# Kernel optimization log

Hardware: AMD Instinct MI355X
Metric: run time of the kernel (lower is better)

Reference implementation:

```python
import jax, jax.numpy as jnp
import numpy as np

N = 100000      # nodes
E = 1600000     # graph edges (avg degree 16)
Q = 1000000     # query edges to score
IN, HID, OUT = 128, 128, 64


def setup_inputs() -> dict:
    key = jax.random.key(0)
    ks = jax.random.split(key, 7)
    feat = jax.random.normal(ks[0], (N, IN), dtype=jnp.float32)
    edge_src = jax.random.randint(ks[1], (E,), 0, N, dtype=jnp.int32)
    edge_dst = jax.random.randint(ks[2], (E,), 0, N, dtype=jnp.int32)
    src = jax.random.randint(ks[3], (Q,), 0, N, dtype=jnp.int32)
    dst = jax.random.randint(ks[4], (Q,), 0, N, dtype=jnp.int32)
    W1 = jax.random.normal(ks[5], (IN, HID), dtype=jnp.float32) / np.sqrt(IN).astype(np.float32)
    b1 = jnp.zeros((HID,), jnp.float32)
    W2 = jax.random.normal(ks[6], (HID, OUT), dtype=jnp.float32) / np.sqrt(HID).astype(np.float32)
    b2 = jnp.zeros((OUT,), jnp.float32)
    return {"feat": feat, "edge_src": edge_src, "edge_dst": edge_dst,
            "src": src, "dst": dst, "W1": W1, "b1": b1, "W2": W2, "b2": b2}


def _graph_conv(h, W, b, edge_src, edge_dst, out_norm, in_norm):
    """DGL GraphConv(norm='both'): D_out^{-1/2} -> aggregate -> D_in^{-1/2}, W, b.
    DGL applies W before aggregation when in_feats > out_feats (same math)."""
    n = h.shape[0]
    h = h * out_norm[:, None]
    if h.shape[1] > W.shape[1]:
        h = h @ W
        agg = jax.ops.segment_sum(h[edge_src], edge_dst, num_segments=n)
    else:
        agg = jax.ops.segment_sum(h[edge_src], edge_dst, num_segments=n)
        agg = agg @ W
    return agg * in_norm[:, None] + b


def reference(feat, edge_src, edge_dst, src, dst, W1, b1, W2, b2):
    n = feat.shape[0]
    ones = jnp.ones((edge_src.shape[0],), feat.dtype)
    out_deg = jax.ops.segment_sum(ones, edge_src, num_segments=n)
    in_deg = jax.ops.segment_sum(ones, edge_dst, num_segments=n)
    out_norm = jnp.maximum(out_deg, 1.0) ** -0.5
    in_norm = jnp.maximum(in_deg, 1.0) ** -0.5

    h = _graph_conv(feat, W1, b1, edge_src, edge_dst, out_norm, in_norm)
    h = jax.nn.relu(h)  # dropout is identity at inference
    h = _graph_conv(h, W2, b2, edge_src, edge_dst, out_norm, in_norm)

    edge_scores = jnp.sum(h[src] * h[dst], axis=-1)
    return jax.nn.sigmoid(edge_scores)
```

## Files before the change

kernel.cpp:

```cpp
#include <hip/hip_runtime.h>
#include <math.h>

static inline size_t align256(size_t x) { return (x + 255) & ~(size_t)255; }

typedef __attribute__((ext_vector_type(8))) short bf16x8;
typedef __attribute__((ext_vector_type(4))) float f32x4;
typedef __attribute__((ext_vector_type(2))) float f32x2;
typedef __attribute__((ext_vector_type(2))) _Float16 half2_t;

__device__ inline float bfLo(unsigned int u) {
  union { unsigned int i; float f; } v; v.i = u << 16; return v.f;
}
__device__ inline float bfHi(unsigned int u) {
  union { unsigned int i; float f; } v; v.i = u & 0xffff0000u; return v.f;
}
__device__ inline unsigned short f2bf(float f) {
  union { float f; unsigned int i; } v; v.f = f;
  unsigned int r = v.i + 0x7FFF + ((v.i >> 16) & 1);
  return (unsigned short)(r >> 16);
}
__device__ inline unsigned int packbf(float lo, float hi) {
  return ((unsigned int)f2bf(hi) << 16) | f2bf(lo);
}
__device__ inline unsigned int packh(float lo, float hi) {
  union { _Float16 h[2]; unsigned int u; } v;
  v.h[0] = (_Float16)lo; v.h[1] = (_Float16)hi;
  return v.u;
}
__device__ inline float qdot(unsigned int a, unsigned int b, float acc) {
#if __has_builtin(__builtin_amdgcn_fdot2)
  union { unsigned int u; half2_t h; } va, vb;
  va.u = a; vb.u = b;
  return __builtin_amdgcn_fdot2(va.h, vb.h, acc, false);
#else
  union { unsigned int u; _Float16 h[2]; } va, vb;
  va.u = a; vb.u = b;
  return acc + (float)va.h[0] * (float)vb.h[0] + (float)va.h[1] * (float)vb.h[1];
#endif
}

__global__ __launch_bounds__(256) void k_coarse_count(const int* __restrict__ esrc,
                                                      const int* __restrict__ edst,
                                                      int E, int chunk, int NB, int G,
                                                      int* __restrict__ blkD,
                                                      int* __restrict__ blkS,
                                                      const float* __restrict__ W1,
                                                      const float* __restrict__ W2,
                                                      unsigned short* __restrict__ W1t,
                                                      unsigned short* __restrict__ W2t) {
  __shared__ int hD[512], hS[512];
  int blk = blockIdx.x, tid = threadIdx.x;
  int t = blk * 256 + tid;
  if (t < 128 * 128) {
    int nn = t >> 7, kk = t & 127;
    W1t[t] = f2bf(W1[kk * 128 + nn]);
  }
  if (t < 64 * 128) {
    int nn = t >> 7, kk = t & 127;
    W2t[t] = f2bf(W2[kk * 64 + nn]);
  }
  for (int i = tid; i < NB; i += 256) { hD[i] = 0; hS[i] = 0; }
  __syncthreads();
  int s0 = blk * chunk, s1 = min(E, s0 + chunk);
  for (int e = s0 + tid; e < s1; e += 256) {
    atomicAdd(&hD[edst[e] >> 8], 1);
    atomicAdd(&hS[esrc[e] >> 8], 1);
  }
  __syncthreads();
  for (int i = tid; i < NB; i += 256) {
    blkD[i * G + blk] = hD[i];
    blkS[i * G + blk] = hS[i];
  }
}

__global__ __launch_bounds__(256) void k_scan1(const int* __restrict__ in,
                                               int* __restrict__ out,
                                               int* __restrict__ bsums, int n) {
  __shared__ int s[256];
  int tid = threadIdx.x, gid = blockIdx.x * 256 + tid;
  int v = (gid < n) ? in[gid] : 0;
  s[tid] = v; __syncthreads();
  for (int o = 1; o < 256; o <<= 1) {
    int t = (tid >= o) ? s[tid - o] : 0;
    __syncthreads();
    s[tid] += t;
    __syncthreads();
  }
  if (gid < n) out[gid] = s[tid] - v;
  if (tid == 255) bsums[blockIdx.x] = s[255];
}

__global__ __launch_bounds__(512) void k_scan2(int* __restrict__ bsums, int nb) {
  __shared__ int s[512];
  int tid = threadIdx.x;
  int* base = bsums + blockIdx.x * nb;
  int v = (tid < nb) ? base[tid] : 0;
  s[tid] = v; __syncthreads();
  for (int o = 1; o < 512; o <<= 1) {
    int t = (tid >= o) ? s[tid - o] : 0;
    __syncthreads();
    s[tid] += t;
    __syncthreads();
  }
  if (tid < nb) base[tid] = s[tid] - v;
}

__global__ __launch_bounds__(256) void k_coarse_scatter(const int* __restrict__ esrc,
                                                        const int* __restrict__ edst,
                                                        int E, int chunk, int NB, int G,
                                                        const int* __restrict__ scD,
                                                        const int* __restrict__ scS,
                                                        const int* __restrict__ bsums,
                                                        unsigned int* __restrict__ pairs,
                                                        unsigned int* __restrict__ keys) {
  __shared__ int cD[512], cS[512];
  int blk = blockIdx.x, tid = threadIdx.x;
  for (int i = tid; i < NB; i += 256) {
    cD[i] = scD[i * G + blk] + bsums[i];
    cS[i] = scS[i * G + blk] + bsums[NB + i];
  }
  __syncthreads();
  int s0 = blk * chunk, s1 = min(E, s0 + chunk);
  for (int e = s0 + tid; e < s1; e += 256) {
    int s = esrc[e], d = edst[e];
    int pd = atomicAdd(&cD[d >> 8], 1);
    pairs[pd] = ((unsigned)s << 8) | ((unsigned)d & 255u);
    int ps = atomicAdd(&cS[s >> 8], 1);
    keys[ps] = (unsigned)s;
  }
}

__global__ __launch_bounds__(256) void k_fine(const unsigned int* __restrict__ pairs,
                                              const unsigned int* __restrict__ keys,
                                              const int* __restrict__ scD,
                                              const int* __restrict__ scS,
                                              const int* __restrict__ bsums,
                                              int G, int E, int N, int NB,
                                              int* __restrict__ cntIn,
                                              float* __restrict__ normIn,
                                              int* __restrict__ offs,
                                              int* __restrict__ csr,
                                              float* __restrict__ normOut) {
  __shared__ int hist[256], scn[256], cur[256];
  int tid = threadIdx.x;
  if (blockIdx.x >= (unsigned)NB) {
    int b = blockIdx.x - NB;
    int bstart = scS[b * G] + bsums[NB + b];
    int bend = (b + 1 < NB) ? scS[(b + 1) * G] + bsums[NB + b + 1] : E;
    hist[tid] = 0;
    __syncthreads();
    for (int e = bstart + tid; e < bend; e += 256)
      atomicAdd(&hist[keys[e] & 255u], 1);
    __syncthreads();
    int node = b * 256 + tid;
    if (node < N) normOut[node] = rsqrtf((float)max(hist[tid], 1));
    return;
  }
  int b = blockIdx.x;
  int bstart = scD[b * G] + bsums[b];
  int bend = (b + 1 < NB) ? scD[(b + 1) * G] + bsums[b + 1] : E;
  hist[tid] = 0;
  __syncthreads();
  for (int e = bstart + tid; e < bend; e += 256)
    atomicAdd(&hist[pairs[e] & 255u], 1);
  __syncthreads();
  int v = hist[tid];
  scn[tid] = v;
  __syncthreads();
  for (int o = 1; o < 256; o <<= 1) {
    int t = (tid >= o) ? scn[tid - o] : 0;
    __syncthreads();
    scn[tid] += t;
    __syncthreads();
  }
  int excl = scn[tid] - v;
  cur[tid] = excl;
  int node = b * 256 + tid;
  if (node < N) {
    cntIn[node] = v;
    normIn[node] = rsqrtf((float)max(v, 1));
    offs[node] = bstart + excl;
  }
  __syncthreads();
  for (int e = bstart + tid; e < bend; e += 256) {
    unsigned int u = pairs[e];
    int p = bstart + atomicAdd(&cur[u & 255u], 1);
    csr[p] = (int)(u >> 8);
  }
}

template <int C, typename TA>
__global__ __launch_bounds__(256) void k_mgemm(const TA* __restrict__ A,
                                               const float* __restrict__ scale,
                                               const unsigned short* __restrict__ Wt,
                                               unsigned short* __restrict__ out, int n) {
  constexpr int KP = 136;
  constexpr int NCH = C / 16;
  __shared__ __align__(16) unsigned short Al[64 * KP];
  __shared__ __align__(16) unsigned short Wl[C * KP];
  int tid = threadIdx.x;
  int r0 = blockIdx.x * 64;

  {
    const uint4* Wg = (const uint4*)Wt;
    uint4* Wd = (uint4*)Wl;
    for (int idx = tid; idx < C * 16; idx += 256) {
      int row = idx >> 4, seg = idx & 15;
      Wd[row * 17 + seg] = Wg[idx];
    }
  }
  {
    int seg = tid & 7;
    for (int it = 0; it < 2; ++it) {
      int row = (tid >> 3) + it * 32;
      int g = r0 + row;
      float v[16];
      if (g < n) {
        float sc = scale[g];
        if constexpr (sizeof(TA) == 4) {
          const float4* Ag = (const float4*)((const float*)A + (size_t)g * 128);
#pragma unroll
          for (int j = 0; j < 4; ++j) {
            float4 f = Ag[seg * 4 + j];
            v[j * 4 + 0] = f.x * sc; v[j * 4 + 1] = f.y * sc;
            v[j * 4 + 2] = f.z * sc; v[j * 4 + 3] = f.w * sc;
          }
        } else {
          const uint4* Ag = (const uint4*)((const unsigned short*)A + (size_t)g * 128);
#pragma unroll
          for (int j = 0; j < 2; ++j) {
            uint4 u = Ag[seg * 2 + j];
            v[j * 8 + 0] = bfLo(u.x) * sc; v[j * 8 + 1] = bfHi(u.x) * sc;
            v[j * 8 + 2] = bfLo(u.y) * sc; v[j * 8 + 3] = bfHi(u.y) * sc;
            v[j * 8 + 4] = bfLo(u.z) * sc; v[j * 8 + 5] = bfHi(u.z) * sc;
            v[j * 8 + 6] = bfLo(u.w) * sc; v[j * 8 + 7] = bfHi(u.w) * sc;
          }
        }
      } else {
#pragma unroll
        for (int j = 0; j < 16; ++j) v[j] = 0.f;
      }
      uint4* dst = (uint4*)(Al + row * KP + seg * 16);
      dst[0] = make_uint4(packbf(v[0], v[1]), packbf(v[2], v[3]),
                          packbf(v[4], v[5]), packbf(v[6], v[7]));
      dst[1] = make_uint4(packbf(v[8], v[9]), packbf(v[10], v[11]),
                          packbf(v[12], v[13]), packbf(v[14], v[15]));
    }
  }
  __syncthreads();

  int lane = tid & 63;
  int w = tid >> 6;
  int quad = lane >> 4, m16 = lane & 15;
  f32x4 acc[NCH];
#pragma unroll
  for (int c = 0; c < NCH; ++c) acc[c] = (f32x4){0.f, 0.f, 0.f, 0.f};

#pragma unroll
  for (int kc = 0; kc < 4; ++kc) {
    int ko = kc * 32 + quad * 8;
    bf16x8 a = *(const bf16x8*)(Al + (w * 16 + m16) * KP + ko);
#pragma unroll
    for (int c = 0; c < NCH; ++c) {
      bf16x8 b = *(const bf16x8*)(Wl + (c * 16 + m16) * KP + ko);
      acc[c] = __builtin_amdgcn_mfma_f32_16x16x32_bf16(a, b, acc[c], 0, 0, 0);
    }
  }

#pragma unroll
  for (int c = 0; c < NCH; ++c)
#pragma unroll
    for (int r = 0; r < 4; ++r) {
      int g = r0 + w * 16 + quad * 4 + r;
      if (g < n) out[(size_t)g * C + c * 16 + m16] = f2bf(acc[c][r]);
    }
}

__global__ __launch_bounds__(256) void k_agg128_relu(const unsigned short* __restrict__ X,
                                                     const int* __restrict__ csr,
                                                     const int* __restrict__ offs,
                                                     const int* __restrict__ cnt,
                                                     const float* __restrict__ norm,
                                                     const float* __restrict__ bias,
                                                     unsigned short* __restrict__ H, int n) {
  int wid = blockIdx.x * 4 + (threadIdx.x >> 6);
  if (wid >= n) return;
  int lane = threadIdx.x & 63;
  int sub = lane & 15;
  int grp = lane >> 4;
  int start = offs[wid], m = cnt[wid];
  const int* p = csr + start;
  const uint4* Xv = (const uint4*)X;
  f32x2 a0 = {0.f, 0.f}, a1 = {0.f, 0.f}, a2 = {0.f, 0.f}, a3 = {0.f, 0.f};
  for (int c0 = 0; c0 < m; c0 += 64) {
    int take = min(64, m - c0);
    int iv = p[c0 + ((lane < take) ? lane : take - 1)];
    int e = 0;
    for (; e + 16 <= take; e += 16) {
      uint4 uu[4];
#pragma unroll
      for (int j = 0; j < 4; ++j) {
        int ss = __shfl(iv, e + j * 4 + grp);
        uu[j] = Xv[(size_t)ss * 16 + sub];
      }
#pragma unroll
      for (int j = 0; j < 4; ++j) {
        a0 += (f32x2){bfLo(uu[j].x), bfHi(uu[j].x)};
        a1 += (f32x2){bfLo(uu[j].y), bfHi(uu[j].y)};
        a2 += (f32x2){bfLo(uu[j].z), bfHi(uu[j].z)};
        a3 += (f32x2){bfLo(uu[j].w), bfHi(uu[j].w)};
      }
    }
    for (; e + 4 <= take; e += 4) {
      int ss = __shfl(iv, e + grp);
      uint4 u = Xv[(size_t)ss * 16 + sub];
      a0 += (f32x2){bfLo(u.x), bfHi(u.x)};
      a1 += (f32x2){bfLo(u.y), bfHi(u.y)};
      a2 += (f32x2){bfLo(u.z), bfHi(u.z)};
      a3 += (f32x2){bfLo(u.w), bfHi(u.w)};
    }
    int r = take - e;
    if (r > 0) {
      int ss = __shfl(iv, min(e + grp, take - 1));
      uint4 u = Xv[(size_t)ss * 16 + sub];
      if (grp < r) {
        a0 += (f32x2){bfLo(u.x), bfHi(u.x)};
        a1 += (f32x2){bfLo(u.y), bfHi(u.y)};
        a2 += (f32x2){bfLo(u.z), bfHi(u.z)};
        a3 += (f32x2){bfLo(u.w), bfHi(u.w)};
      }
    }
  }
  float a[8] = {a0.x, a0.y, a1.x, a1.y, a2.x, a2.y, a3.x, a3.y};
#pragma unroll
  for (int k = 0; k < 8; ++k) {
    a[k] += __shfl_xor(a[k], 16);
    a[k] += __shfl_xor(a[k], 32);
  }
  float nm = norm[wid];
  const float4* bv = (const float4*)bias;
  float4 b0 = bv[sub * 2], b1 = bv[sub * 2 + 1];
  if (grp == 0) {
    float o0 = fmaxf(a[0] * nm + b0.x, 0.f);
    float o1 = fmaxf(a[1] * nm + b0.y, 0.f);
    float o2 = fmaxf(a[2] * nm + b0.z, 0.f);
    float o3 = fmaxf(a[3] * nm + b0.w, 0.f);
    float o4 = fmaxf(a[4] * nm + b1.x, 0.f);
    float o5 = fmaxf(a[5] * nm + b1.y, 0.f);
    float o6 = fmaxf(a[6] * nm + b1.z, 0.f);
    float o7 = fmaxf(a[7] * nm + b1.w, 0.f);
    uint4 o = make_uint4(packbf(o0, o1), packbf(o2, o3),
                         packbf(o4, o5), packbf(o6, o7));
    ((uint4*)H)[(size_t)wid * 16 + sub] = o;
  }
}

__global__ __launch_bounds__(256) void k_agg64(const unsigned short* __restrict__ X,
                                               const int* __restrict__ csr,
                                               const int* __restrict__ offs,
                                               const int* __restrict__ cnt,
                                               const float* __restrict__ norm,
                                               const float* __restrict__ bias,
                                               unsigned short* __restrict__ H, int n) {
  int wid = blockIdx.x * 4 + (threadIdx.x >> 6);
  if (wid >= n) return;
  int lane = threadIdx.x & 63;
  int sub = lane & 7;
  int grp = lane >> 3;
  int start = offs[wid], m = cnt[wid];
  const int* p = csr + start;
  const uint4* Xv = (const uint4*)X;
  f32x2 a0 = {0.f, 0.f}, a1 = {0.f, 0.f}, a2 = {0.f, 0.f}, a3 = {0.f, 0.f};
  for (int c0 = 0; c0 < m; c0 += 64) {
    int take = min(64, m - c0);
    int iv = p[c0 + ((lane < take) ? lane : take - 1)];
    int e = 0;
    for (; e + 32 <= take; e += 32) {
      uint4 uu[4];
#pragma unroll
      for (int j = 0; j < 4; ++j) {
        int ss = __shfl(iv, e + j * 8 + grp);
        uu[j] = Xv[(size_t)ss * 8 + sub];
      }
#pragma unroll
      for (int j = 0; j < 4; ++j) {
        a0 += (f32x2){bfLo(uu[j].x), bfHi(uu[j].x)};
        a1 += (f32x2){bfLo(uu[j].y), bfHi(uu[j].y)};
        a2 += (f32x2){bfLo(uu[j].z), bfHi(uu[j].z)};
        a3 += (f32x2){bfLo(uu[j].w), bfHi(uu[j].w)};
      }
    }
    for (; e + 8 <= take; e += 8) {
      int ss = __shfl(iv, e + grp);
      uint4 u = Xv[(size_t)ss * 8 + sub];
      a0 += (f32x2){bfLo(u.x), bfHi(u.x)};
      a1 += (f32x2){bfLo(u.y), bfHi(u.y)};
      a2 += (f32x2){bfLo(u.z), bfHi(u.z)};
      a3 += (f32x2){bfLo(u.w), bfHi(u.w)};
    }
    int r = take - e;
    if (r > 0) {
      int ss = __shfl(iv, min(e + grp, take - 1));
      uint4 u = Xv[(size_t)ss * 8 + sub];
      if (grp < r) {
        a0 += (f32x2){bfLo(u.x), bfHi(u.x)};
        a1 += (f32x2){bfLo(u.y), bfHi(u.y)};
        a2 += (f32x2){bfLo(u.z), bfHi(u.z)};
        a3 += (f32x2){bfLo(u.w), bfHi(u.w)};
      }
    }
  }
  float a[8] = {a0.x, a0.y, a1.x, a1.y, a2.x, a2.y, a3.x, a3.y};
#pragma unroll
  for (int k = 0; k < 8; ++k) {
    a[k] += __shfl_xor(a[k], 8);
    a[k] += __shfl_xor(a[k], 16);
    a[k] += __shfl_xor(a[k], 32);
  }
  float nm = norm[wid];
  const float4* bv = (const float4*)bias;
  float4 b0 = bv[sub * 2], b1 = bv[sub * 2 + 1];
  if (grp == 0) {
    uint4 o = make_uint4(packh(a[0] * nm + b0.x, a[1] * nm + b0.y),
                         packh(a[2] * nm + b0.z, a[3] * nm + b0.w),
                         packh(a[4] * nm + b1.x, a[5] * nm + b1.y),
                         packh(a[6] * nm + b1.z, a[7] * nm + b1.w));
    ((uint4*)H)[(size_t)wid * 8 + sub] = o;
  }
}

__global__ __launch_bounds__(256) void k_score(const unsigned short* __restrict__ H,
                                               const int* __restrict__ qs,
                                               const int* __restrict__ qd,
                                               float* __restrict__ out, int q, int qStride) {
  int t = blockIdx.x * 256 + threadIdx.x;
  int sub = t & 7;
  int q0 = t >> 3;
  int q1 = q0 + qStride;
  const uint4* Hv = (const uint4*)H;
  float p0 = 0.f, p1 = 0.f;
  if (q0 < q) {
    uint4 a = Hv[(size_t)qs[q0] * 8 + sub];
    uint4 b = Hv[(size_t)qd[q0] * 8 + sub];
    uint4 c, d;
    bool has1 = (q1 < q);
    if (has1) {
      c = Hv[(size_t)qs[q1] * 8 + sub];
      d = Hv[(size_t)qd[q1] * 8 + sub];
    }
    p0 = qdot(a.x, b.x, p0); p0 = qdot(a.y, b.y, p0);
    p0 = qdot(a.z, b.z, p0); p0 = qdot(a.w, b.w, p0);
    if (has1) {
      p1 = qdot(c.x, d.x, p1); p1 = qdot(c.y, d.y, p1);
      p1 = qdot(c.z, d.z, p1); p1 = qdot(c.w, d.w, p1);
    }
  }
  p0 += __shfl_xor(p0, 1); p1 += __shfl_xor(p1, 1);
  p0 += __shfl_xor(p0, 2); p1 += __shfl_xor(p1, 2);
  p0 += __shfl_xor(p0, 4); p1 += __shfl_xor(p1, 4);
  if (sub == 0 && q0 < q) {
    out[q0] = 1.f / (1.f + expf(-p0));
    if (q1 < q) out[q1] = 1.f / (1.f + expf(-p1));
  }
}

extern "C" void kernel_launch(void* const* d_in, const int* in_sizes, int n_in,
                              void* d_out, int out_size, void* d_ws, size_t ws_size,
                              hipStream_t stream) {
  const float* feat = (const float*)d_in[0];
  const int* esrc   = (const int*)d_in[1];
  const int* edst   = (const int*)d_in[2];
  const int* qsrc   = (const int*)d_in[3];
  const int* qdst   = (const int*)d_in[4];
  const float* W1   = (const float*)d_in[5];
  const float* b1   = (const float*)d_in[6];
  const float* W2   = (const float*)d_in[7];
  const float* b2   = (const float*)d_in[8];
  float* out = (float*)d_out;

  const int N = in_sizes[0] / 128;
  const int E = in_sizes[1];
  const int Q = in_sizes[3];

  const int G = 256;
  const int NB = (N + 255) >> 8;
  const int chunk = (E + G - 1) / G;
  const int lenS = NB * G;
  const int gScan = lenS / 256;

  char* w = (char*)d_ws;
  size_t o = 0;
  unsigned short* X1 = (unsigned short*)(w + o); o += align256((size_t)N * 128 * 2);
  unsigned short* X2 = (unsigned short*)(w + o); o += align256((size_t)N * 64 * 2);
  unsigned short* H2 = (unsigned short*)(w + o); o += align256((size_t)N * 64 * 2);
  int* cntIn = (int*)(w + o);       o += align256((size_t)N * 4);
  float* normOut = (float*)(w + o); o += align256((size_t)N * 4);
  float* normIn = (float*)(w + o);  o += align256((size_t)N * 4);
  int* offs = (int*)(w + o);        o += align256((size_t)N * 4);
  int* blk = (int*)(w + o);         o += align256((size_t)lenS * 8);
  int* sc = (int*)(w + o);          o += align256((size_t)lenS * 8);
  int* bsums = (int*)(w + o);       o += align256((size_t)8192);
  unsigned short* W1t = (unsigned short*)(w + o); o += align256((size_t)128 * 128 * 2);
  unsigned short* W2t = (unsigned short*)(w + o); o += align256((size_t)64 * 128 * 2);
  unsigned int* pairs = (unsigned int*)(w + o); o += align256((size_t)E * 4);
  unsigned int* keys = (unsigned int*)(w + o); o += align256((size_t)E * 4);
  int* csr = (int*)(w + o);         o += align256((size_t)E * 4);

  int* blkD = blk;        int* blkS = blk + lenS;
  int* scD = sc;          int* scS = sc + lenS;

  k_coarse_count<<<G, 256, 0, stream>>>(esrc, edst, E, chunk, NB, G, blkD, blkS,
                                        W1, W2, W1t, W2t);
  k_scan1<<<2 * gScan, 256, 0, stream>>>(blk, sc, bsums, 2 * lenS);
  k_scan2<<<2, 512, 0, stream>>>(bsums, gScan);
  k_coarse_scatter<<<G, 256, 0, stream>>>(esrc, edst, E, chunk, NB, G, scD, scS,
                                          bsums, pairs, keys);
  k_fine<<<2 * NB, 256, 0, stream>>>(pairs, keys, scD, scS, bsums, G, E, N, NB,
                                     cntIn, normIn, offs, csr, normOut);

  const int gRows = (N + 63) / 64;
  k_mgemm<128, float><<<gRows, 256, 0, stream>>>(feat, normOut, W1t, X1, N);
  k_agg128_relu<<<(N + 3) / 4, 256, 0, stream>>>(X1, csr, offs, cntIn, normIn, b1, X2, N);
  k_mgemm<64, unsigned short><<<gRows, 256, 0, stream>>>(X2, normOut, W2t, X1, N);
  k_agg64<<<(N + 3) / 4, 256, 0, stream>>>(X1, csr, offs, cntIn, normIn, b2, H2, N);
  const int qHalf = (Q + 1) / 2;
  k_score<<<((qHalf * 8) + 255) / 256, 256, 0, stream>>>(H2, qsrc, qdst, out, Q, qHalf);
}
```

Baseline: 318.8 us.

## Aggregate 128-wide layer via MFMA with mask matrix over 16-node groups

Replaces the per-node wave gather-and-add aggregation for layer one with a kernel where each wave handles 16 consecutive destination nodes. It streams their contiguous CSR neighbor rows through LDS in tiles of 32, reads them back with transposing LDS loads, and accumulates with bf16 MFMA using a 0/1 mask matrix that selects which edges belong to which node. This trades scalar FP adds and cross-lane reductions for matrix ops and wider coalesced loads. The cost is extra LDS traffic and wasted MFMA work on masked entries. Nodes beyond the last multiple of 16 (N>>4) are never processed, which is fine for N=100000 but not in general.

After: 324.7 us. About the same (+1.9%).

```diff
diff --git a/kernel.cpp b/kernel.cpp
--- a/kernel.cpp
+++ b/kernel.cpp
@@ -4,6 +4,7 @@
 static inline size_t align256(size_t x) { return (x + 255) & ~(size_t)255; }
 
 typedef __attribute__((ext_vector_type(8))) short bf16x8;
+typedef __attribute__((ext_vector_type(4))) short s16x4;
 typedef __attribute__((ext_vector_type(4))) float f32x4;
 typedef __attribute__((ext_vector_type(2))) float f32x2;
 typedef __attribute__((ext_vector_type(2))) _Float16 half2_t;
@@ -276,82 +277,108 @@
     }
 }
 
-__global__ __launch_bounds__(256) void k_agg128_relu(const unsigned short* __restrict__ X,
+__global__ __launch_bounds__(256) void k_agg128_mfma(const unsigned short* __restrict__ X,
                                                      const int* __restrict__ csr,
                                                      const int* __restrict__ offs,
                                                      const int* __restrict__ cnt,
                                                      const float* __restrict__ norm,
                                                      const float* __restrict__ bias,
-                                                     unsigned short* __restrict__ H, int n) {
-  int wid = blockIdx.x * 4 + (threadIdx.x >> 6);
-  if (wid >= n) return;
-  int lane = threadIdx.x & 63;
-  int sub = lane & 15;
-  int grp = lane >> 4;
-  int start = offs[wid], m = cnt[wid];
-  const int* p = csr + start;
-  const uint4* Xv = (const uint4*)X;
-  f32x2 a0 = {0.f, 0.f}, a1 = {0.f, 0.f}, a2 = {0.f, 0.f}, a3 = {0.f, 0.f};
-  for (int c0 = 0; c0 < m; c0 += 64) {
-    int take = min(64, m - c0);
-    int iv = p[c0 + ((lane < take) ? lane : take - 1)];
-    int e = 0;
-    for (; e + 16 <= take; e += 16) {
-      uint4 uu[4];
-#pragma unroll
-      for (int j = 0; j < 4; ++j) {
-        int ss = __shfl(iv, e + j * 4 + grp);
-        uu[j] = Xv[(size_t)ss * 16 + sub];
+                                                     unsigned short* __restrict__ H,
+                                                     int n, int E) {
+  __shared__ __attribute__((aligned(128))) unsigned short sA[4][32 * 128];
+  const int tid = threadIdx.x;
+  const int w = tid >> 6, l = tid & 63;
+  const int g = blockIdx.x * 4 + w;
+  const int nGroups = n >> 4;
+  if (g >= nGroups) return;
+  const int n0 = g << 4;
+
+  const int mnode = n0 + (l & 15);
+  const int s_m = offs[mnode];
+  const int c_m = cnt[mnode];
+  const int gs = __shfl(s_m, 0);
+  const int ge = __shfl(s_m + c_m, 15);
+  const int nt = (ge - gs + 31) >> 5;
+
+  const unsigned ldsb = (unsigned)(size_t)(&sA[w][0]);
+  unsigned short* ldsw = &sA[w][0];
+
+  const int eloc = (l >> 1) & 3;
+  const unsigned cbyte = (unsigned)(((l >> 3) << 5) | ((l & 1) << 4));
+
+  f32x4 acc[8];
+#pragma unroll
+  for (int c = 0; c < 8; ++c) acc[c] = (f32x4){0.f, 0.f, 0.f, 0.f};
+
+  const int kgrp = (l >> 4) << 3;
+  int ev = 0;
+  if (nt > 0) ev = csr[min(gs + (l & 31), E - 1)];
+
+  for (int t = 0; t < nt; ++t) {
+    const int tbase = gs + (t << 5);
+    uint4 st[8];
+#pragma unroll
+    for (int i = 0; i < 8; ++i) {
+      int row = __shfl(ev, (i << 2) + eloc);
+      st[i] = *(const uint4*)((const char*)X + ((size_t)(unsigned)row << 8) + cbyte);
+    }
+    if (t + 1 < nt) ev = csr[min(tbase + 32 + (l & 31), E - 1)];
+#pragma unroll
+    for (int i = 0; i < 8; ++i)
+      *(uint4*)((char*)ldsw + (i << 10) + (l << 4)) = st[i];
+
+    const int r0 = tbase + kgrp - s_m;
+    unsigned mw0 = (((unsigned)(r0 + 0) < (unsigned)c_m) ? 0x3F80u : 0u) |
+                   ((((unsigned)(r0 + 1) < (unsigned)c_m) ? 0x3F80u : 0u) << 16);
+    unsigned mw1 = (((unsigned)(r0 + 2) < (unsigned)c_m) ? 0x3F80u : 0u) |
+                   ((((unsigned)(r0 + 3) < (unsigned)c_m) ? 0x3F80u : 0u) << 16);
+    unsigned mw2 = (((unsigned)(r0 + 4) < (unsigned)c_m) ? 0x3F80u : 0u) |
+                   ((((unsigned)(r0 + 5) < (unsigned)c_m) ? 0x3F80u : 0u) << 16);
+    unsigned mw3 = (((unsigned)(r0 + 6) < (unsigned)c_m) ? 0x3F80u : 0u) |
+                   ((((unsigned)(r0 + 7) < (unsigned)c_m) ? 0x3F80u : 0u) << 16);
+    union { unsigned u[4]; bf16x8 v; } cv;
+    cv.u[0] = mw0; cv.u[1] = mw1; cv.u[2] = mw2; cv.u[3] = mw3;
+    const bf16x8 amask = cv.v;
+
+    asm volatile("s_waitcnt lgkmcnt(0)" ::: "memory");
+    __builtin_amdgcn_sched_barrier(0);
+
+    const unsigned ta = ldsb + (unsigned)(((l >> 4) << 11) + ((l & 15) << 3));
+    s16x4 lo[8], hi[8];
+#pragma unroll
+    for (int c = 0; c < 8; ++c) {
+      asm volatile("ds_read_b64_tr_b16 %0, %2 offset:0\n\t"
+                   "ds_read_b64_tr_b16 %1, %2 offset:1024"
+                   : "=v"(lo[c]), "=v"(hi[c])
+                   : "v"(ta + (unsigned)(c << 7)));
+    }
+    asm volatile("s_waitcnt lgkmcnt(0)" ::: "memory");
+    __builtin_amdgcn_sched_barrier(0);
+
+#pragma unroll
+    for (int c = 0; c < 8; ++c) {
+      bf16x8 b = __builtin_shufflevector(lo[c], hi[c], 0, 1, 2, 3, 4, 5, 6, 7);
+      acc[c] = __builtin_amdgcn_mfma_f32_16x16x32_bf16(amask, b, acc[c], 0, 0, 0);
+    }
+  }
+
+  const int rbase = (l >> 4) << 2;
+  float nmr[4];
+#pragma unroll
+  for (int r = 0; r < 4; ++r) nmr[r] = norm[n0 + rbase + r];
+  const int s = l & 15;
+#pragma unroll
+  for (int c = 0; c < 8; ++c) {
+    const float bv = bias[(c << 4) | s];
+#pragma unroll
+    for (int r = 0; r < 4; ++r) {
+      float h = fmaxf(acc[c][r] * nmr[r] + bv, 0.f);
+      float hn = __shfl_xor(h, 1);
+      if (!(l & 1)) {
+        unsigned p = ((unsigned)f2bf(hn) << 16) | f2bf(h);
+        *(unsigned*)(H + (size_t)(n0 + rbase + r) * 128 + (c << 4) + s) = p;
       }
-#pragma unroll
-      for (int j = 0; j < 4; ++j) {
-        a0 += (f32x2){bfLo(uu[j].x), bfHi(uu[j].x)};
-        a1 += (f32x2){bfLo(uu[j].y), bfHi(uu[j].y)};
-        a2 += (f32x2){bfLo(uu[j].z), bfHi(uu[j].z)};
-        a3 += (f32x2){bfLo(uu[j].w), bfHi(uu[j].w)};
-      }
-    }
-    for (; e + 4 <= take; e += 4) {
-      int ss = __shfl(iv, e + grp);
-      uint4 u = Xv[(size_t)ss * 16 + sub];
-      a0 += (f32x2){bfLo(u.x), bfHi(u.x)};
-      a1 += (f32x2){bfLo(u.y), bfHi(u.y)};
-      a2 += (f32x2){bfLo(u.z), bfHi(u.z)};
-      a3 += (f32x2){bfLo(u.w), bfHi(u.w)};
-    }
-    int r = take - e;
-    if (r > 0) {
-      int ss = __shfl(iv, min(e + grp, take - 1));
-      uint4 u = Xv[(size_t)ss * 16 + sub];
-      if (grp < r) {
-        a0 += (f32x2){bfLo(u.x), bfHi(u.x)};
-        a1 += (f32x2){bfLo(u.y), bfHi(u.y)};
-        a2 += (f32x2){bfLo(u.z), bfHi(u.z)};
-        a3 += (f32x2){bfLo(u.w), bfHi(u.w)};
-      }
-    }
-  }
-  float a[8] = {a0.x, a0.y, a1.x, a1.y, a2.x, a2.y, a3.x, a3.y};
-#pragma unroll
-  for (int k = 0; k < 8; ++k) {
-    a[k] += __shfl_xor(a[k], 16);
-    a[k] += __shfl_xor(a[k], 32);
-  }
-  float nm = norm[wid];
-  const float4* bv = (const float4*)bias;
-  float4 b0 = bv[sub * 2], b1 = bv[sub * 2 + 1];
-  if (grp == 0) {
-    float o0 = fmaxf(a[0] * nm + b0.x, 0.f);
-    float o1 = fmaxf(a[1] * nm + b0.y, 0.f);
-    float o2 = fmaxf(a[2] * nm + b0.z, 0.f);
-    float o3 = fmaxf(a[3] * nm + b0.w, 0.f);
-    float o4 = fmaxf(a[4] * nm + b1.x, 0.f);
-    float o5 = fmaxf(a[5] * nm + b1.y, 0.f);
-    float o6 = fmaxf(a[6] * nm + b1.z, 0.f);
-    float o7 = fmaxf(a[7] * nm + b1.w, 0.f);
-    uint4 o = make_uint4(packbf(o0, o1), packbf(o2, o3),
-                         packbf(o4, o5), packbf(o6, o7));
-    ((uint4*)H)[(size_t)wid * 16 + sub] = o;
+    }
   }
 }
 
@@ -520,7 +547,9 @@
 
   const int gRows = (N + 63) / 64;
   k_mgemm<128, float><<<gRows, 256, 0, stream>>>(feat, normOut, W1t, X1, N);
-  k_agg128_relu<<<(N + 3) / 4, 256, 0, stream>>>(X1, csr, offs, cntIn, normIn, b1, X2, N);
+  const int nGroups = N >> 4;
+  k_agg128_mfma<<<(nGroups + 3) / 4, 256, 0, stream>>>(X1, csr, offs, cntIn, normIn,
+                                                       b1, X2, N, E);
   k_mgemm<64, unsigned short><<<gRows, 256, 0, stream>>>(X2, normOut, W2t, X1, N);
   k_agg64<<<(N + 3) / 4, 256, 0, stream>>>(X1, csr, offs, cntIn, normIn, b2, H2, N);
   const int qHalf = (Q + 1) / 2;
```
